# Kernel tuning notes

Measured on AMD Instinct MI355X. Metric: run time of the kernel, lower is better.

Reference implementation:

```python
import jax, jax.numpy as jnp
import numpy as np

DIM = 768
HEADS = 12
B, N = 1, 4096


def setup_inputs() -> dict:
    key = jax.random.key(0)
    k1, k2, k3 = jax.random.split(key, 3)
    x = jax.random.normal(k1, (B, N, DIM), dtype=jnp.float32)
    W_qkv = jax.random.normal(k2, (DIM, 3 * DIM), dtype=jnp.float32) * (DIM ** -0.5)
    W_out = jax.random.normal(k3, (DIM, DIM), dtype=jnp.float32) * (DIM ** -0.5)
    b_out = jnp.zeros((DIM,), dtype=jnp.float32)
    return {"x": x, "W_qkv": W_qkv, "W_out": W_out, "b_out": b_out}


def reference(x, W_qkv, W_out, b_out):
    b, n, dim = x.shape
    h = HEADS
    d = dim // h
    qkv = x @ W_qkv  # [b, n, 3*dim]
    q, k, v = jnp.split(qkv, 3, axis=-1)
    # 'b n (h d) -> b h n d'
    def to_heads(a):
        return a.reshape(b, n, h, d).transpose(0, 2, 1, 3)
    q, k, v = to_heads(q), to_heads(k), to_heads(v)
    # NOTE: original module computes self.scale but never applies it -> unscaled dots
    dots = jnp.einsum('bhid,bhjd->bhij', q, k)
    attn = jax.nn.softmax(dots, axis=-1)
    out = jnp.einsum('bhij,bhjd->bhid', attn, v)
    out = out.transpose(0, 2, 1, 3).reshape(b, n, dim)  # 'b h n d -> b n (h d)'
    return out @ W_out + b_out
```

## Files before the change

kernel.cpp:

```cpp
#include <hip/hip_runtime.h>

typedef unsigned short ushort_t;
typedef unsigned int uint_t;
typedef __bf16 bf16x8 __attribute__((ext_vector_type(8)));
typedef __bf16 bf16x4 __attribute__((ext_vector_type(4)));
typedef float f32x4 __attribute__((ext_vector_type(4)));
typedef ushort_t u16x4 __attribute__((ext_vector_type(4)));

#define NSEQ 4096
#define DIMM 768
#define NQKV 2304
#define HEADS 12
#define LOG2E 1.4426950408889634f

#if __has_builtin(__builtin_amdgcn_exp2f)
#define EXP2(x) __builtin_amdgcn_exp2f(x)
#else
#define EXP2(x) exp2f(x)
#endif


__device__ __forceinline__ ushort_t f2bf(float f) {
    uint_t u = __float_as_uint(f);
    u = u + 0x7fffu + ((u >> 16) & 1u);
    return (ushort_t)(u >> 16);
}
__device__ __forceinline__ f32x4 zero4() {
    f32x4 v = {0.f, 0.f, 0.f, 0.f};
    return v;
}

__device__ __forceinline__ void gload_lds16(const ushort_t* g, ushort_t* l) {
    __builtin_amdgcn_global_load_lds(
        (const __attribute__((address_space(1))) void*)g,
        (__attribute__((address_space(3))) void*)l, 16, 0, 0);
}

__device__ __forceinline__ void pack_w_tile(const float* __restrict__ src,
                                            ushort_t* __restrict__ dst,
                                            int K, int N, int bk, int bn, int t,
                                            ushort_t* Ls) {
    const int tr = t >> 4, tc = t & 15;
#pragma unroll
    for (int i = 0; i < 4; ++i) {
        int r = tr + 16 * i;
        float4 v = *(const float4*)(&src[(size_t)(bk + r) * N + bn + tc * 4]);
        const float* vv = (const float*)&v;
#pragma unroll
        for (int j = 0; j < 4; ++j) Ls[(tc * 4 + j) * 72 + r] = f2bf(vv[j]);
    }
    __syncthreads();
    const int KB = K >> 3;
    const int n = t >> 2;
    const int ks = t & 3;
    const int gn = bn + n;
    size_t base = ((size_t)(gn >> 4) * KB + ((bk + ks * 16) >> 3)) * 128 + (gn & 15) * 8;
    *(uint4*)(&dst[base])       = *(const uint4*)(&Ls[n * 72 + ks * 16]);
    *(uint4*)(&dst[base + 128]) = *(const uint4*)(&Ls[n * 72 + ks * 16 + 8]);
}

#define CVT_BLOCKS   3072
#define PW1_BLOCKS   (12 * 36)
#define PW2_BLOCKS   (12 * 12)

__global__ __launch_bounds__(256) void prep_kernel(
    const float* __restrict__ X, const float* __restrict__ Wqkv, const float* __restrict__ Wout,
    ushort_t* __restrict__ Ap, ushort_t* __restrict__ Wqp, ushort_t* __restrict__ Wop)
{
    __shared__ ushort_t Ls[64 * 72];
    const int b = blockIdx.x;
    const int t = threadIdx.x;
    if (b < CVT_BLOCKS) {
        int i = b * 256 + t;
        int row = i / (DIMM / 4);
        int k0 = (i - row * (DIMM / 4)) * 4;
        float4 v = *(const float4*)(&X[(size_t)row * DIMM + k0]);
        u16x4 p = { f2bf(v.x), f2bf(v.y), f2bf(v.z), f2bf(v.w) };
        size_t idx = ((size_t)(row >> 4) * (DIMM / 8) + (k0 >> 3)) * 128 + (row & 15) * 8 + (k0 & 7);
        *(u16x4*)(&Ap[idx]) = p;
    } else if (b < CVT_BLOCKS + PW1_BLOCKS) {
        int j = b - CVT_BLOCKS;
        pack_w_tile(Wqkv, Wqp, DIMM, NQKV, (j % 12) * 64, (j / 12) * 64, t, Ls);
    } else {
        int j = b - CVT_BLOCKS - PW1_BLOCKS;
        pack_w_tile(Wout, Wop, DIMM, DIMM, (j % 12) * 64, (j / 12) * 64, t, Ls);
    }
}

#define QKV_LOAD(af, bfv, kt) do {                                                            \
    _Pragma("unroll")                                                                         \
    for (int mi = 0; mi < 4; ++mi)                                                            \
        af[mi] = *(const bf16x8*)(&Ap[((size_t)(amb + mi) * KB + (kt) * 4 + g) * 128 + m16 * 8]); \
    _Pragma("unroll")                                                                         \
    for (int nj = 0; nj < 4; ++nj)                                                            \
        bfv[nj] = *(const bf16x8*)(&Bp[((size_t)(bnb + nj) * KB + (kt) * 4 + g) * 128 + m16 * 8]); \
} while (0)

__global__ __launch_bounds__(256) void qkv_gemm_kernel(
    const ushort_t* __restrict__ Ap, const ushort_t* __restrict__ Bp,
    ushort_t* __restrict__ Qp, ushort_t* __restrict__ Kp, ushort_t* __restrict__ Vp)
{
    const int t = threadIdx.x;
    const int lane = t & 63;
    const int w = t >> 6;
    const int m16 = lane & 15;
    const int g = lane >> 4;
    const int wrow = (w >> 1) * 64;
    const int wcol = (w & 1) * 64;
    const int bm = blockIdx.y * 128;
    const int bn = blockIdx.x * 128;
    const int amb = (bm + wrow) >> 4;
    const int bnb = (bn + wcol) >> 4;
    const int KB = DIMM / 8;
    const int which = bn / DIMM;

    f32x4 acc[4][4];
#pragma unroll
    for (int i = 0; i < 4; ++i)
#pragma unroll
        for (int j = 0; j < 4; ++j) acc[i][j] = zero4();

    bf16x8 af0[4], bf0[4], af1[4], bf1[4];
    QKV_LOAD(af0, bf0, 0);

    if (which < 2) {
        for (int kt = 0; kt < 24; kt += 2) {
            QKV_LOAD(af1, bf1, kt + 1);
#pragma unroll
            for (int mi = 0; mi < 4; ++mi)
#pragma unroll
                for (int nj = 0; nj < 4; ++nj)
                    acc[mi][nj] = __builtin_amdgcn_mfma_f32_16x16x32_bf16(bf0[nj], af0[mi], acc[mi][nj], 0, 0, 0);
            if (kt + 2 < 24) QKV_LOAD(af0, bf0, kt + 2);
#pragma unroll
            for (int mi = 0; mi < 4; ++mi)
#pragma unroll
                for (int nj = 0; nj < 4; ++nj)
                    acc[mi][nj] = __builtin_amdgcn_mfma_f32_16x16x32_bf16(bf1[nj], af1[mi], acc[mi][nj], 0, 0, 0);
        }
        ushort_t* dst = (which == 0) ? Qp : Kp;
        const float scale = (which == 0) ? LOG2E : 1.0f;
        const int cb = bn - which * DIMM + wcol;
        const int h = cb >> 6;
        const int ghi = g >> 1, glo = g & 1;
#pragma unroll
        for (int mi = 0; mi < 4; ++mi) {
            int sblk = amb + mi;
#pragma unroll
            for (int nj = 0; nj < 4; ++nj) {
                size_t idx = (((size_t)h * 256 + sblk) * 8 + nj * 2 + ghi) * 128 + m16 * 8 + glo * 4;
                u16x4 pk = { f2bf(acc[mi][nj][0] * scale), f2bf(acc[mi][nj][1] * scale),
                             f2bf(acc[mi][nj][2] * scale), f2bf(acc[mi][nj][3] * scale) };
                *(u16x4*)(&dst[idx]) = pk;
            }
        }
    } else {
        for (int kt = 0; kt < 24; kt += 2) {
            QKV_LOAD(af1, bf1, kt + 1);
#pragma unroll
            for (int mi = 0; mi < 4; ++mi)
#pragma unroll
                for (int nj = 0; nj < 4; ++nj)
                    acc[mi][nj] = __builtin_amdgcn_mfma_f32_16x16x32_bf16(af0[mi], bf0[nj], acc[mi][nj], 0, 0, 0);
            if (kt + 2 < 24) QKV_LOAD(af0, bf0, kt + 2);
#pragma unroll
            for (int mi = 0; mi < 4; ++mi)
#pragma unroll
                for (int nj = 0; nj < 4; ++nj)
                    acc[mi][nj] = __builtin_amdgcn_mfma_f32_16x16x32_bf16(af1[mi], bf1[nj], acc[mi][nj], 0, 0, 0);
        }
        const int cb = bn - 2 * DIMM + wcol;
        const int h = cb >> 6;
        const int ghi = g >> 1, glo = g & 1;
        const int kb8 = (bm + wrow) >> 3;
#pragma unroll
        for (int mi = 0; mi < 4; ++mi) {
#pragma unroll
            for (int nj = 0; nj < 4; ++nj) {
                size_t idx = (((size_t)h * 512 + kb8 + mi * 2 + ghi) * 4 + nj) * 128 + m16 * 8 + glo * 4;
                u16x4 pk = { f2bf(acc[mi][nj][0]), f2bf(acc[mi][nj][1]),
                             f2bf(acc[mi][nj][2]), f2bf(acc[mi][nj][3]) };
                *(u16x4*)(&Vp[idx]) = pk;
            }
        }
    }
}

#define ATTN_STAGE() do {                                  \
    _Pragma("unroll")                                      \
    for (int j = 0; j < 4; ++j)                            \
        gload_lds16(kp + j * 512, &KVs[w][j * 512]);       \
    _Pragma("unroll")                                      \
    for (int j = 0; j < 4; ++j)                            \
        gload_lds16(vp + j * 128, &KVs[w][2048 + j * 512]);\
    kp += 2048; vp += 2048;                                \
} while (0)

__global__ __launch_bounds__(128, 3) void attn_kernel(
    const ushort_t* __restrict__ Qp, const ushort_t* __restrict__ Kp,
    const ushort_t* __restrict__ Vp, float* __restrict__ Opart, float* __restrict__ Lpart,
    int niter)
{
    __shared__ ushort_t KVs[2][4096];
    __shared__ ushort_t Ps[2][64 * 40];
    const int t = threadIdx.x;
    const int lane = t & 63;
    const int w = t >> 6;
    const int m16 = lane & 15;
    const int g = lane >> 4;
    const int h = blockIdx.y;
    const int half = blockIdx.z;
    const int qb = blockIdx.x * 128 + w * 64;
    const int qblk0 = qb >> 4;
    const int kblk0 = half * niter * 4;
    const int vblk0 = half * niter * 8;

    bf16x8 qf[4][2];
#pragma unroll
    for (int mi = 0; mi < 4; ++mi)
#pragma unroll
        for (int kd = 0; kd < 2; ++kd)
            qf[mi][kd] = *(const bf16x8*)(&Qp[(((size_t)h * 256 + qblk0 + mi) * 8 + kd * 4 + g) * 128 + m16 * 8]);

    const ushort_t* kp = Kp + ((size_t)h * 256 + kblk0) * 1024 + g * 128 + m16 * 8;
    const ushort_t* vp = Vp + ((size_t)h * 512 + vblk0) * 512 + g * 512 + m16 * 8;

    f32x4 oacc[4][4];
#pragma unroll
    for (int mi = 0; mi < 4; ++mi)
#pragma unroll
        for (int dj = 0; dj < 4; ++dj) oacc[mi][dj] = zero4();
    f32x4 lacc[4] = {zero4(), zero4(), zero4(), zero4()};

    const int nsteps = niter * 2;
    ATTN_STAGE();

    const int lb = lane * 8;
    for (int s = 0; s < nsteps; ++s) {
        asm volatile("s_waitcnt vmcnt(0)" ::: "memory");
        bf16x8 kf[2][2], vf[4];
        kf[0][0] = *(const bf16x8*)(&KVs[w][lb]);
        kf[0][1] = *(const bf16x8*)(&KVs[w][512 + lb]);
        kf[1][0] = *(const bf16x8*)(&KVs[w][1024 + lb]);
        kf[1][1] = *(const bf16x8*)(&KVs[w][1536 + lb]);
#pragma unroll
        for (int dj = 0; dj < 4; ++dj)
            vf[dj] = *(const bf16x8*)(&KVs[w][2048 + dj * 512 + lb]);
        asm volatile("s_waitcnt lgkmcnt(0)" ::: "memory");
        if (s + 1 < nsteps) ATTN_STAGE();

#pragma unroll
        for (int mi = 0; mi < 4; ++mi) {
#pragma unroll
            for (int nj = 0; nj < 2; ++nj) {
                f32x4 st = zero4();
                st = __builtin_amdgcn_mfma_f32_16x16x32_bf16(kf[nj][0], qf[mi][0], st, 0, 0, 0);
                st = __builtin_amdgcn_mfma_f32_16x16x32_bf16(kf[nj][1], qf[mi][1], st, 0, 0, 0);
                f32x4 p;
#pragma unroll
                for (int r = 0; r < 4; ++r) p[r] = EXP2(st[r]);
                lacc[mi] += p;
                bf16x4 pk = { (__bf16)p[0], (__bf16)p[1], (__bf16)p[2], (__bf16)p[3] };
                *(bf16x4*)(&Ps[w][(mi * 16 + m16) * 40 + nj * 16 + g * 4]) = pk;
            }
            bf16x8 pf = *(const bf16x8*)(&Ps[w][(mi * 16 + m16) * 40 + g * 8]);
#pragma unroll
            for (int dj = 0; dj < 4; ++dj)
                oacc[mi][dj] = __builtin_amdgcn_mfma_f32_16x16x32_bf16(pf, vf[dj], oacc[mi][dj], 0, 0, 0);
        }
    }

    float* Oph = Opart + (size_t)half * NSEQ * DIMM;
    float* Lph = Lpart + (size_t)half * HEADS * NSEQ + (size_t)h * NSEQ;
#pragma unroll
    for (int mi = 0; mi < 4; ++mi) {
        float l = (lacc[mi][0] + lacc[mi][1]) + (lacc[mi][2] + lacc[mi][3]);
        l += __shfl_xor(l, 16);
        l += __shfl_xor(l, 32);
        if (g == 0) Lph[qb + mi * 16 + m16] = l;
    }
#pragma unroll
    for (int mi = 0; mi < 4; ++mi) {
#pragma unroll
        for (int r = 0; r < 4; ++r) {
            int row = qb + mi * 16 + g * 4 + r;
#pragma unroll
            for (int dj = 0; dj < 4; ++dj)
                Oph[(size_t)row * DIMM + h * 64 + dj * 16 + m16] = oacc[mi][dj][r];
        }
    }
}

__global__ __launch_bounds__(256) void merge_kernel(
    const float* __restrict__ Opart, const float* __restrict__ Lpart,
    ushort_t* __restrict__ Xap, int nsplit)
{
    int i = blockIdx.x * 256 + threadIdx.x;
    int row = i / (DIMM / 4);
    int col0 = (i - row * (DIMM / 4)) * 4;
    int h = col0 >> 6;
    float l = 0.f;
    f32x4 o = zero4();
    for (int s = 0; s < nsplit; ++s) {
        l += Lpart[(size_t)s * HEADS * NSEQ + (size_t)h * NSEQ + row];
        f32x4 ov = *(const f32x4*)(&Opart[(size_t)s * NSEQ * DIMM + (size_t)row * DIMM + col0]);
        o += ov;
    }
    float inv = 1.0f / l;
    u16x4 p = { f2bf(o[0] * inv), f2bf(o[1] * inv), f2bf(o[2] * inv), f2bf(o[3] * inv) };
    size_t idx = ((size_t)(row >> 4) * (DIMM / 8) + (col0 >> 3)) * 128 + (row & 15) * 8 + (col0 & 7);
    *(u16x4*)(&Xap[idx]) = p;
}

__global__ __launch_bounds__(64, 4) void out_gemm_kernel(
    const ushort_t* __restrict__ Ap, const ushort_t* __restrict__ Bp,
    const float* __restrict__ bias, float* __restrict__ out)
{
    const int lane = threadIdx.x & 63;
    const int m16 = lane & 15;
    const int g = lane >> 4;
    const int bm = blockIdx.y * 32;
    const int bn = blockIdx.x * 64;
    const int amb = bm >> 4;
    const int bnb = bn >> 4;
    const int KB = DIMM / 8;

    f32x4 acc[2][4];
#pragma unroll
    for (int i = 0; i < 2; ++i)
#pragma unroll
        for (int j = 0; j < 4; ++j) acc[i][j] = zero4();

#pragma unroll 2
    for (int kt = 0; kt < 24; ++kt) {
        bf16x8 af[2], bfv[4];
#pragma unroll
        for (int mi = 0; mi < 2; ++mi)
            af[mi] = *(const bf16x8*)(&Ap[((size_t)(amb + mi) * KB + kt * 4 + g) * 128 + m16 * 8]);
#pragma unroll
        for (int nj = 0; nj < 4; ++nj)
            bfv[nj] = *(const bf16x8*)(&Bp[((size_t)(bnb + nj) * KB + kt * 4 + g) * 128 + m16 * 8]);
#pragma unroll
        for (int mi = 0; mi < 2; ++mi)
#pragma unroll
            for (int nj = 0; nj < 4; ++nj)
                acc[mi][nj] = __builtin_amdgcn_mfma_f32_16x16x32_bf16(af[mi], bfv[nj], acc[mi][nj], 0, 0, 0);
    }
#pragma unroll
    for (int mi = 0; mi < 2; ++mi) {
#pragma unroll
        for (int nj = 0; nj < 4; ++nj) {
            int col = bn + nj * 16 + m16;
            float bv = bias[col];
#pragma unroll
            for (int r = 0; r < 4; ++r) {
                int row = bm + mi * 16 + g * 4 + r;
                out[(size_t)row * DIMM + col] = acc[mi][nj][r] + bv;
            }
        }
    }
}

extern "C" void kernel_launch(void* const* d_in, const int* in_sizes, int n_in,
                              void* d_out, int out_size, void* d_ws, size_t ws_size,
                              hipStream_t stream) {
    (void)in_sizes; (void)n_in; (void)out_size;
    const float* X    = (const float*)d_in[0];
    const float* Wqkv = (const float*)d_in[1];
    const float* Wout = (const float*)d_in[2];
    const float* bout = (const float*)d_in[3];
    float* out = (float*)d_out;

    const size_t TSZ = (size_t)NSEQ * DIMM;
    const size_t fixed = TSZ * 2 * 5 + (size_t)NQKV * DIMM * 2 + (size_t)DIMM * DIMM * 2;
    const size_t per_split = TSZ * 4 + (size_t)HEADS * NSEQ * 4;
    const int nsplit = (ws_size >= fixed + 4 * per_split) ? 4 : 2;

    unsigned char* p = (unsigned char*)d_ws;
    ushort_t* Ap  = (ushort_t*)p; p += TSZ * 2;
    ushort_t* Wqp = (ushort_t*)p; p += (size_t)NQKV * DIMM * 2;
    ushort_t* Wop = (ushort_t*)p; p += (size_t)DIMM * DIMM * 2;
    ushort_t* Qp  = (ushort_t*)p; p += TSZ * 2;
    ushort_t* Kp  = (ushort_t*)p; p += TSZ * 2;
    ushort_t* Vp  = (ushort_t*)p; p += TSZ * 2;
    ushort_t* Xap = (ushort_t*)p; p += TSZ * 2;
    float* Opart  = (float*)p;    p += (size_t)nsplit * TSZ * 4;
    float* Lpart  = (float*)p;

    const int niter = (NSEQ / 64) / nsplit;

    prep_kernel<<<CVT_BLOCKS + PW1_BLOCKS + PW2_BLOCKS, 256, 0, stream>>>(X, Wqkv, Wout, Ap, Wqp, Wop);
    qkv_gemm_kernel<<<dim3(NQKV / 128, NSEQ / 128), 256, 0, stream>>>(Ap, Wqp, Qp, Kp, Vp);
    attn_kernel<<<dim3(NSEQ / 128, HEADS, nsplit), 128, 0, stream>>>(Qp, Kp, Vp, Opart, Lpart, niter);
    merge_kernel<<<TSZ / 4 / 256, 256, 0, stream>>>(Opart, Lpart, Xap, nsplit);
    out_gemm_kernel<<<dim3(DIMM / 64, NSEQ / 32), 64, 0, stream>>>(Xap, Wop, bout, out);
}
```

Measured before the change: 202.6 us.

## Share K/V tiles across four waves per block with cooperative double-buffered loads

Result: faster. 195.9 us (-3.3%).

```diff
diff --git a/kernel.cpp b/kernel.cpp
--- a/kernel.cpp
+++ b/kernel.cpp
@@ -186,23 +186,13 @@
     }
 }
 
-#define ATTN_STAGE() do {                                  \
-    _Pragma("unroll")                                      \
-    for (int j = 0; j < 4; ++j)                            \
-        gload_lds16(kp + j * 512, &KVs[w][j * 512]);       \
-    _Pragma("unroll")                                      \
-    for (int j = 0; j < 4; ++j)                            \
-        gload_lds16(vp + j * 128, &KVs[w][2048 + j * 512]);\
-    kp += 2048; vp += 2048;                                \
-} while (0)
-
-__global__ __launch_bounds__(128, 3) void attn_kernel(
+__global__ __launch_bounds__(256, 3) void attn_kernel(
     const ushort_t* __restrict__ Qp, const ushort_t* __restrict__ Kp,
     const ushort_t* __restrict__ Vp, float* __restrict__ Opart, float* __restrict__ Lpart,
     int niter)
 {
-    __shared__ ushort_t KVs[2][4096];
-    __shared__ ushort_t Ps[2][64 * 40];
+    __shared__ ushort_t KV[2][4096];
+    __shared__ ushort_t Ps[4][64 * 40];
     const int t = threadIdx.x;
     const int lane = t & 63;
     const int w = t >> 6;
@@ -210,7 +200,7 @@
     const int g = lane >> 4;
     const int h = blockIdx.y;
     const int half = blockIdx.z;
-    const int qb = blockIdx.x * 128 + w * 64;
+    const int qb = blockIdx.x * 256 + w * 64;
     const int qblk0 = qb >> 4;
     const int kblk0 = half * niter * 4;
     const int vblk0 = half * niter * 8;
@@ -222,8 +212,11 @@
         for (int kd = 0; kd < 2; ++kd)
             qf[mi][kd] = *(const bf16x8*)(&Qp[(((size_t)h * 256 + qblk0 + mi) * 8 + kd * 4 + g) * 128 + m16 * 8]);
 
-    const ushort_t* kp = Kp + ((size_t)h * 256 + kblk0) * 1024 + g * 128 + m16 * 8;
-    const ushort_t* vp = Vp + ((size_t)h * 512 + vblk0) * 512 + g * 512 + m16 * 8;
+    const ushort_t* src = ((w < 2)
+        ? Kp + ((size_t)h * 256 + kblk0) * 1024
+        : Vp + ((size_t)h * 512 + vblk0) * 512)
+        + (w & 1) * 1024 + lane * 8;
+    const int ldso = (w >> 1) * 2048 + (w & 1) * 1024;
 
     f32x4 oacc[4][4];
 #pragma unroll
@@ -233,21 +226,28 @@
     f32x4 lacc[4] = {zero4(), zero4(), zero4(), zero4()};
 
     const int nsteps = niter * 2;
-    ATTN_STAGE();
-
-    const int lb = lane * 8;
+    gload_lds16(src, &KV[0][ldso]);
+    gload_lds16(src + 512, &KV[0][ldso + 512]);
+    src += 2048;
+
     for (int s = 0; s < nsteps; ++s) {
-        asm volatile("s_waitcnt vmcnt(0)" ::: "memory");
+        __syncthreads();
+        if (s + 1 < nsteps) {
+            ushort_t* d = &KV[(s + 1) & 1][ldso];
+            gload_lds16(src, d);
+            gload_lds16(src + 512, d + 512);
+            src += 2048;
+        }
+        const ushort_t* kb = &KV[s & 1][g * 128 + m16 * 8];
+        const ushort_t* vb = &KV[s & 1][2048 + g * 512 + m16 * 8];
         bf16x8 kf[2][2], vf[4];
-        kf[0][0] = *(const bf16x8*)(&KVs[w][lb]);
-        kf[0][1] = *(const bf16x8*)(&KVs[w][512 + lb]);
-        kf[1][0] = *(const bf16x8*)(&KVs[w][1024 + lb]);
-        kf[1][1] = *(const bf16x8*)(&KVs[w][1536 + lb]);
+        kf[0][0] = *(const bf16x8*)(kb);
+        kf[0][1] = *(const bf16x8*)(kb + 512);
+        kf[1][0] = *(const bf16x8*)(kb + 1024);
+        kf[1][1] = *(const bf16x8*)(kb + 1536);
 #pragma unroll
         for (int dj = 0; dj < 4; ++dj)
-            vf[dj] = *(const bf16x8*)(&KVs[w][2048 + dj * 512 + lb]);
-        asm volatile("s_waitcnt lgkmcnt(0)" ::: "memory");
-        if (s + 1 < nsteps) ATTN_STAGE();
+            vf[dj] = *(const bf16x8*)(vb + dj * 128);
 
 #pragma unroll
         for (int mi = 0; mi < 4; ++mi) {
@@ -391,7 +391,7 @@
 
     prep_kernel<<<CVT_BLOCKS + PW1_BLOCKS + PW2_BLOCKS, 256, 0, stream>>>(X, Wqkv, Wout, Ap, Wqp, Wop);
     qkv_gemm_kernel<<<dim3(NQKV / 128, NSEQ / 128), 256, 0, stream>>>(Ap, Wqp, Qp, Kp, Vp);
-    attn_kernel<<<dim3(NSEQ / 128, HEADS, nsplit), 128, 0, stream>>>(Qp, Kp, Vp, Opart, Lpart, niter);
+    attn_kernel<<<dim3(NSEQ / 256, HEADS, nsplit), 256, 0, stream>>>(Qp, Kp, Vp, Opart, Lpart, niter);
     merge_kernel<<<TSZ / 4 / 256, 256, 0, stream>>>(Opart, Lpart, Xap, nsplit);
     out_gemm_kernel<<<dim3(DIMM / 64, NSEQ / 32), 64, 0, stream>>>(Xap, Wop, bout, out);
 }
```
